# Optimization experiments

Hardware: AMD Instinct MI355X
Metric: run time of the kernel (lower is better)

## Reference

```python
import jax, jax.numpy as jnp
import numpy as np

VW, VD, VH = 96, 96, 96  # voxel_width, voxel_depth, voxel_height


def _grid_points():
    # voxel centers mapped to [-1, 1]: (2*i + 1 - N) / N
    xp = (2.0 * jnp.arange(VW) + 1.0 - VW) / VW
    yp = (2.0 * jnp.arange(VD) + 1.0 - VD) / VD
    zp = (2.0 * jnp.arange(VH) + 1.0 - VH) / VH
    X, Y, Z = jnp.meshgrid(xp, yp, zp, indexing='ij')
    return jnp.stack([X.ravel(), Y.ravel(), Z.ravel()], axis=-1)  # (V, 3)


def setup_inputs() -> dict:
    key = jax.random.key(0)
    k1, k2 = jax.random.split(key)
    B, NV, NF = 8, 2048, 512
    vertices = jax.random.uniform(k1, (B, NV, 3), dtype=jnp.float32, minval=-1.0, maxval=1.0)
    facets = jax.random.randint(k2, (B, NF, 4), 0, NV, dtype=jnp.int64)
    return {"vertices": vertices, "facets": facets}


def reference(vertices, facets):
    # vertices: (B, NV, 3) float32; facets: (B, NF, 4) int indices into vertices
    B = vertices.shape[0]
    NF = facets.shape[1]
    # vertices_to_facets: per-batch gather -> (B, NF, 4, 3)
    fverts = jax.vmap(lambda v, f: v[f])(vertices, facets)
    P = _grid_points()                      # (V, 3) voxel centers
    V = P.shape[0]

    def step(idx_map, xs):
        fi, verts = xs                      # verts: (B, 4, 3)
        v3 = verts[:, 3]                    # (B, 3)
        # T[:, j] = verts[j] - verts[3]  (columns are tetra edges)
        T = jnp.swapaxes(verts[:, :3] - v3[:, None, :], 1, 2)  # (B, 3, 3)
        a, b, c = T[:, 0, 0], T[:, 0, 1], T[:, 0, 2]
        d, e, f = T[:, 1, 0], T[:, 1, 1], T[:, 1, 2]
        g, h, i = T[:, 2, 0], T[:, 2, 1], T[:, 2, 2]
        # adjugate of T (matches t_inv_* in the original)
        adj = jnp.stack([
            jnp.stack([e * i - f * h, c * h - b * i, b * f - c * e], axis=-1),
            jnp.stack([f * g - d * i, a * i - c * g, c * d - a * f], axis=-1),
            jnp.stack([d * h - e * g, b * g - a * h, a * e - b * d], axis=-1),
        ], axis=1)                          # (B, 3, 3)
        det = a * (e * i - f * h) - b * (d * i - f * g) + c * (d * h - e * g)  # (B,)
        dvec = P[None, :, :] - v3[:, None, :]                  # (B, V, 3)
        lam = jnp.einsum('brc,bvc->bvr', adj, dvec) / det[:, None, None]  # (B, V, 3)
        lam4 = 1.0 - lam.sum(axis=-1, keepdims=True)
        lams = jnp.concatenate([lam, lam4], axis=-1)           # (B, V, 4)
        # original skips when any lambda < 0 or > 1 (strict) -> inside is inclusive
        inside = jnp.all((lams >= 0.0) & (lams <= 1.0), axis=-1)  # (B, V)
        idx_map = jnp.where((idx_map < 0) & inside, fi, idx_map)
        return idx_map, None

    idx0 = jnp.full((B, V), -1, dtype=jnp.int32)
    xs = (jnp.arange(NF, dtype=jnp.int32), jnp.swapaxes(fverts, 0, 1))
    idx_map, _ = jax.lax.scan(step, idx0, xs)
    alpha = (idx_map >= 0).astype(jnp.float32).reshape(B, VW, VD, VH)
    return alpha
```

## Files before the change

kernel.cpp:

```cpp
#include <hip/hip_runtime.h>

#pragma clang fp contract(off)

#define VWD 96
#define NVERT 2048
#define NFAC 512
#define NBATCH 8
#define NSLAB 3456
#define RECF 16
#define CULC 22

#define CUL(c, b, f) cul[(size_t)(c) * (NBATCH * NFAC) + (size_t)(b) * NFAC + (f)]

__global__ __launch_bounds__(512) void precompute_kernel(
    const float* __restrict__ vertices,
    const int*   __restrict__ facets,
    float*       __restrict__ cul,
    float*       __restrict__ body)
{
    __shared__ unsigned skey[NFAC];
    const int b = blockIdx.x;
    const int j = threadIdx.x;
    const float* vb = vertices + (size_t)b * NVERT * 3;

    int4 fi = ((const int4*)facets)[b * NFAC + j];
    float x0 = vb[3*fi.x+0], y0 = vb[3*fi.x+1], z0 = vb[3*fi.x+2];
    float x1 = vb[3*fi.y+0], y1 = vb[3*fi.y+1], z1 = vb[3*fi.y+2];
    float x2 = vb[3*fi.z+0], y2 = vb[3*fi.z+1], z2 = vb[3*fi.z+2];
    float x3 = vb[3*fi.w+0], y3 = vb[3*fi.w+1], z3 = vb[3*fi.w+2];
    float a  = x0-x3, bb = x1-x3, c  = x2-x3;
    float d  = y0-y3, e  = y1-y3, f  = y2-y3;
    float g  = z0-z3, h  = z1-z3, ii = z2-z3;
    float A00 = e*ii - f*h,  A01 = c*h  - bb*ii, A02 = bb*f - c*e;
    float A10 = f*g  - d*ii, A11 = a*ii - c*g,   A12 = c*d  - a*f;
    float A20 = d*h  - e*g,  A21 = bb*g - a*h,   A22 = a*e  - bb*d;
    float det = a*(e*ii - f*h) - bb*(d*ii - f*g) + c*(d*h - e*g);
    if (det < 0.0f) {
        det = -det;
        A00 = -A00; A01 = -A01; A02 = -A02;
        A10 = -A10; A11 = -A11; A12 = -A12;
        A20 = -A20; A21 = -A21; A22 = -A22;
    }
    unsigned myk = ~__float_as_uint(det);
    skey[j] = myk;
    __syncthreads();

    int rank = 0;
    const uint4* sk4 = (const uint4*)skey;
    for (int k0 = 0; k0 < NFAC; k0 += 4) {
        uint4 kk = sk4[k0 >> 2];
        rank += (kk.x < myk) + ((kk.x == myk) & (k0 + 0 < j));
        rank += (kk.y < myk) + ((kk.y == myk) & (k0 + 1 < j));
        rank += (kk.z < myk) + ((kk.z == myk) & (k0 + 2 < j));
        rank += (kk.w < myk) + ((kk.w == myk) & (k0 + 3 < j));
    }

    CUL(0, b, rank) = fminf(fminf(x0,x1),fminf(x2,x3)) - 1e-4f;
    CUL(1, b, rank) = fminf(fminf(y0,y1),fminf(y2,y3)) - 1e-4f;
    CUL(2, b, rank) = fminf(fminf(z0,z1),fminf(z2,z3)) - 1e-4f;
    CUL(3, b, rank) = fmaxf(fmaxf(x0,x1),fmaxf(x2,x3)) + 1e-4f;
    CUL(4, b, rank) = fmaxf(fmaxf(y0,y1),fmaxf(y2,y3)) + 1e-4f;
    CUL(5, b, rank) = fmaxf(fmaxf(z0,z1),fmaxf(z2,z3)) + 1e-4f;

    const float HX = 7.0f/96.0f, HZ = 3.0f/96.0f;
    auto plane = [&](float pax, float pay, float paz,
                     float pbx, float pby, float pbz,
                     float pcx, float pcy, float pcz,
                     float pox, float poy, float poz, int base) {
        float e1x = pbx-pax, e1y = pby-pay, e1z = pbz-paz;
        float e2x = pcx-pax, e2y = pcy-pay, e2z = pcz-paz;
        float nx = e1y*e2z - e1z*e2y;
        float ny = e1z*e2x - e1x*e2z;
        float nz = e1x*e2y - e1y*e2x;
        float sdot = nx*(pox-pax) + ny*(poy-pay) + nz*(poz-paz);
        if (sdot > 0.0f) { nx=-nx; ny=-ny; nz=-nz; sdot=-sdot; }
        float dpl = nx*pax + ny*pay + nz*paz;
        float n1s = fabsf(nx)+fabsf(ny)+fabsf(nz);
        float M = 1e-4f*(-sdot) + 1e-4f*n1s + 1e-4f;
        float rhs = dpl + M + (fabsf(nx)*HX + fabsf(ny)*HX + fabsf(nz)*HZ);
        CUL(base+0, b, rank) = nx;
        CUL(base+1, b, rank) = ny;
        CUL(base+2, b, rank) = nz;
        CUL(base+3, b, rank) = rhs;
    };
    plane(x1,y1,z1, x2,y2,z2, x3,y3,z3, x0,y0,z0, 6);
    plane(x0,y0,z0, x2,y2,z2, x3,y3,z3, x1,y1,z1, 10);
    plane(x0,y0,z0, x1,y1,z1, x3,y3,z3, x2,y2,z2, 14);
    plane(x0,y0,z0, x1,y1,z1, x2,y2,z2, x3,y3,z3, 18);

    float* bo = body + ((size_t)b * NFAC + rank) * RECF;
    bo[0]  = det; bo[1]  = x3;  bo[2]  = y3;  bo[3]  = z3;
    bo[4]  = A00; bo[5]  = A01; bo[6]  = A02;
    bo[7]  = A10; bo[8]  = A11; bo[9]  = A12;
    bo[10] = A20; bo[11] = A21; bo[12] = A22;
    bo[13] = det * (1.0f - 1e-5f) - 1e-25f;
    bo[14] = det * (1.0f + 1e-5f) + 1e-25f;
    bo[15] = 0.0f;
}

__global__ __launch_bounds__(512) void mask_kernel(
    const float* __restrict__ cul,
    unsigned long long* __restrict__ masks)
{
    const int col = blockIdx.x;
    const int b   = blockIdx.y;
    const int f   = threadIdx.x;
    const int w   = threadIdx.x >> 6;
    float bminx=CUL(0,b,f), bminy=CUL(1,b,f), bminz=CUL(2,b,f);
    float bmaxx=CUL(3,b,f), bmaxy=CUL(4,b,f), bmaxz=CUL(5,b,f);
    float n0x=CUL(6,b,f),  n0y=CUL(7,b,f),  n0z=CUL(8,b,f),  r0=CUL(9,b,f);
    float n1x=CUL(10,b,f), n1y=CUL(11,b,f), n1z=CUL(12,b,f), r1=CUL(13,b,f);
    float n2x=CUL(14,b,f), n2y=CUL(15,b,f), n2z=CUL(16,b,f), r2=CUL(17,b,f);
    float n3x=CUL(18,b,f), n3y=CUL(19,b,f), n3z=CUL(20,b,f), r3=CUL(21,b,f);

    const int sx = col / 12, sy = col % 12;
    const float cx = (float)(16*sx + 8 - VWD) / 96.0f;
    const float cy = (float)(16*sy + 8 - VWD) / 96.0f;
    const float colminx = (float)(16*sx + 1  - VWD) / 96.0f;
    const float colmaxx = (float)(16*sx + 15 - VWD) / 96.0f;
    const float colminy = (float)(16*sy + 1  - VWD) / 96.0f;
    const float colmaxy = (float)(16*sy + 15 - VWD) / 96.0f;
    const bool ovxy = (bminx <= colmaxx) & (bmaxx >= colminx) &
                      (bminy <= colmaxy) & (bmaxy >= colminy);

    const float cz0   = (float)(4 - VWD) / 96.0f;
    const float stepc = 8.0f / 96.0f;
    float d0 = n0x*cx + n0y*cy + n0z*cz0 - r0;  float s0 = n0z*stepc;
    float d1 = n1x*cx + n1y*cy + n1z*cz0 - r1;  float s1 = n1z*stepc;
    float d2 = n2x*cx + n2y*cy + n2z*cz0 - r2;  float s2 = n2z*stepc;
    float d3 = n3x*cx + n3y*cy + n3z*cz0 - r3;  float s3 = n3z*stepc;
    float zlo = (float)(1 - VWD) / 96.0f;
    float zhi = (float)(7 - VWD) / 96.0f;

    unsigned long long* mp = masks + ((size_t)b * NSLAB + (size_t)col * 24) * 8 + w;
#pragma unroll 4
    for (int sz = 0; sz < 24; ++sz) {
        bool ov = ovxy & (bminz <= zhi) & (bmaxz >= zlo) &
                  (d0 <= 0.0f) & (d1 <= 0.0f) & (d2 <= 0.0f) & (d3 <= 0.0f);
        unsigned long long bal = __ballot((int)ov);
        if ((threadIdx.x & 63) == 0) mp[(size_t)sz * 8] = bal;
        d0 += s0; d1 += s1; d2 += s2; d3 += s3;
        zlo += stepc; zhi += stepc;
    }
}

__global__ __launch_bounds__(256) void voxelize_kernel(
    const float*              __restrict__ body,
    const unsigned long long* __restrict__ masks,
    float*                    __restrict__ out)
{
    const int b    = blockIdx.y;
    const int wave = threadIdx.x >> 6;
    const int lane = threadIdx.x & 63;
    const int slab = blockIdx.x * 4 + wave;
    const int sz = slab % 24;
    const int sy = (slab / 24) % 12;
    const int sx = slab / 288;
    const int ix  = sx*8 + (lane >> 3);
    const int iy  = sy*8 + (lane & 7);
    const int iz0 = sz*4;

    const float px  = (float)(2*ix + 1 - VWD) / 96.0f;
    const float py  = (float)(2*iy + 1 - VWD) / 96.0f;
    const float pz0 = (float)(2*(iz0+0) + 1 - VWD) / 96.0f;
    const float pz1 = (float)(2*(iz0+1) + 1 - VWD) / 96.0f;
    const float pz2 = (float)(2*(iz0+2) + 1 - VWD) / 96.0f;
    const float pz3 = (float)(2*(iz0+3) + 1 - VWD) / 96.0f;

    const unsigned long long* mp = masks + ((size_t)b * NSLAB + slab) * 8;
    const float* bb = body + (size_t)b * NFAC * RECF;

    unsigned fnd = 0u;
    for (int w = 0; w < 8; ++w) {
        unsigned long long m = mp[w];
        while (m) {
            int bit = __builtin_ctzll(m);
            m &= m - 1;
            int f = __builtin_amdgcn_readfirstlane(w * 64 + bit);
            const float* bo = bb + f * RECF;
            float det = bo[0], v3x = bo[1], v3y = bo[2], v3z = bo[3];
            float A00 = bo[4],  A01 = bo[5],  A02 = bo[6];
            float A10 = bo[7],  A11 = bo[8],  A12 = bo[9];
            float A20 = bo[10], A21 = bo[11], A22 = bo[12];
            float dhi = bo[13], mhi = bo[14];
            float dx = px - v3x, dy = py - v3y;
            float p0 = A00*dx + A01*dy;
            float p1 = A10*dx + A11*dy;
            float p2 = A20*dx + A21*dy;
            float dzk0 = pz0 - v3z, dzk1 = pz1 - v3z;
            float dzk2 = pz2 - v3z, dzk3 = pz3 - v3z;
#pragma unroll
            for (int k = 0; k < 4; ++k) {
                float dzk = (k == 0) ? dzk0 : (k == 1) ? dzk1
                          : (k == 2) ? dzk2 : dzk3;
                float n0 = p0 + A02*dzk;
                float n1 = p1 + A12*dzk;
                float n2 = p2 + A22*dzk;
                float sm = (n0 + n1) + n2;
                float mn = fminf(fminf(n0, n1), n2);
                bool ge0 = (mn >= 0.0f);
                bool def = ge0 & (sm <= dhi);
                bool may = ge0 & (sm <= mhi);
                bool needex = may & !def & !((fnd >> k) & 1u);
                if (__any(needex)) {
                    float l0 = n0 / det;
                    float l1 = n1 / det;
                    float l2 = n2 / det;
                    float l3 = 1.0f - ((l0 + l1) + l2);
                    bool inside = (l0 >= 0.0f) & (l0 <= 1.0f) &
                                  (l1 >= 0.0f) & (l1 <= 1.0f) &
                                  (l2 >= 0.0f) & (l2 <= 1.0f) &
                                  (l3 >= 0.0f) & (l3 <= 1.0f);
                    if (needex & inside) fnd |= (1u << k);
                }
                if (def) fnd |= (1u << k);
            }
            if (__all(fnd == 15u)) goto done;
        }
    }
done:
    float4 v;
    v.x = (fnd & 1u) ? 1.0f : 0.0f;
    v.y = (fnd & 2u) ? 1.0f : 0.0f;
    v.z = (fnd & 4u) ? 1.0f : 0.0f;
    v.w = (fnd & 8u) ? 1.0f : 0.0f;
    *(float4*)&out[(size_t)b*(VWD*VWD*VWD) + (size_t)ix*(VWD*VWD) + iy*VWD + iz0] = v;
}

extern "C" void kernel_launch(void* const* d_in, const int* in_sizes, int n_in,
                              void* d_out, int out_size, void* d_ws, size_t ws_size,
                              hipStream_t stream) {
    const float* vertices = (const float*)d_in[0];
    const int*   facets   = (const int*)d_in[1];
    float*       out      = (float*)d_out;

    float* cul  = (float*)d_ws;
    float* body = (float*)((char*)d_ws + (size_t)CULC * NBATCH * NFAC * 4);
    unsigned long long* msk =
        (unsigned long long*)((char*)d_ws +
                              (size_t)(CULC + RECF) * NBATCH * NFAC * 4);

    precompute_kernel<<<NBATCH, 512, 0, stream>>>(vertices, facets, cul, body);
    mask_kernel<<<dim3(144, NBATCH), 512, 0, stream>>>(cul, msk);
    dim3 grid(NSLAB / 4, NBATCH);
    voxelize_kernel<<<grid, 256, 0, stream>>>(body, msk, out);
}
```

Before: 145.8 us.

## Use persistent voxelize blocks with atomic work-stealing over slab chunks

Replaces the static one-wave-per-slab grid with a fixed grid of 2048 blocks whose waves fetch groups of four slabs from a global atomic counter, reset by the precompute kernel. The goal is to even out load across compute units, since slabs differ widely in how many candidate facets they test. The cost is one atomic per four slabs, extra workspace for the counter, and a dependence on the counter being reset before each launch.

```diff
diff --git a/kernel.cpp b/kernel.cpp
--- a/kernel.cpp
+++ b/kernel.cpp
@@ -7,6 +7,8 @@
 #define NFAC 512
 #define NBATCH 8
 #define NSLAB 3456
+#define NWORK (NSLAB * NBATCH)
+#define GRAIN 4
 #define RECF 16
 #define CULC 22
 
@@ -16,11 +18,13 @@
     const float* __restrict__ vertices,
     const int*   __restrict__ facets,
     float*       __restrict__ cul,
-    float*       __restrict__ body)
+    float*       __restrict__ body,
+    unsigned*    __restrict__ counter)
 {
     __shared__ unsigned skey[NFAC];
     const int b = blockIdx.x;
     const int j = threadIdx.x;
+    if (b == 0 && j == 0) *counter = 0u;
     const float* vb = vertices + (size_t)b * NVERT * 3;
 
     int4 fi = ((const int4*)facets)[b * NFAC + j];
@@ -147,84 +151,98 @@
 __global__ __launch_bounds__(256) void voxelize_kernel(
     const float*              __restrict__ body,
     const unsigned long long* __restrict__ masks,
-    float*                    __restrict__ out)
+    float*                    __restrict__ out,
+    unsigned*                 __restrict__ counter)
 {
-    const int b    = blockIdx.y;
-    const int wave = threadIdx.x >> 6;
     const int lane = threadIdx.x & 63;
-    const int slab = blockIdx.x * 4 + wave;
-    const int sz = slab % 24;
-    const int sy = (slab / 24) % 12;
-    const int sx = slab / 288;
-    const int ix  = sx*8 + (lane >> 3);
-    const int iy  = sy*8 + (lane & 7);
-    const int iz0 = sz*4;
-
-    const float px  = (float)(2*ix + 1 - VWD) / 96.0f;
-    const float py  = (float)(2*iy + 1 - VWD) / 96.0f;
-    const float pz0 = (float)(2*(iz0+0) + 1 - VWD) / 96.0f;
-    const float pz1 = (float)(2*(iz0+1) + 1 - VWD) / 96.0f;
-    const float pz2 = (float)(2*(iz0+2) + 1 - VWD) / 96.0f;
-    const float pz3 = (float)(2*(iz0+3) + 1 - VWD) / 96.0f;
-
-    const unsigned long long* mp = masks + ((size_t)b * NSLAB + slab) * 8;
-    const float* bb = body + (size_t)b * NFAC * RECF;
-
-    unsigned fnd = 0u;
-    for (int w = 0; w < 8; ++w) {
-        unsigned long long m = mp[w];
-        while (m) {
-            int bit = __builtin_ctzll(m);
-            m &= m - 1;
-            int f = __builtin_amdgcn_readfirstlane(w * 64 + bit);
-            const float* bo = bb + f * RECF;
-            float det = bo[0], v3x = bo[1], v3y = bo[2], v3z = bo[3];
-            float A00 = bo[4],  A01 = bo[5],  A02 = bo[6];
-            float A10 = bo[7],  A11 = bo[8],  A12 = bo[9];
-            float A20 = bo[10], A21 = bo[11], A22 = bo[12];
-            float dhi = bo[13], mhi = bo[14];
-            float dx = px - v3x, dy = py - v3y;
-            float p0 = A00*dx + A01*dy;
-            float p1 = A10*dx + A11*dy;
-            float p2 = A20*dx + A21*dy;
-            float dzk0 = pz0 - v3z, dzk1 = pz1 - v3z;
-            float dzk2 = pz2 - v3z, dzk3 = pz3 - v3z;
+
+    for (;;) {
+        unsigned g;
+        if (lane == 0) g = atomicAdd(counter, 1u);
+        g = (unsigned)__builtin_amdgcn_readfirstlane((int)g);
+        if (g >= NWORK / GRAIN) return;
+
+        for (int t = 0; t < GRAIN; ++t) {
+            const unsigned id = g * GRAIN + t;
+            const int b    = id / NSLAB;
+            const int slab = id % NSLAB;
+            const int sz = slab % 24;
+            const int sy = (slab / 24) % 12;
+            const int sx = slab / 288;
+            const int ix  = sx*8 + (lane >> 3);
+            const int iy  = sy*8 + (lane & 7);
+            const int iz0 = sz*4;
+
+            const float px  = (float)(2*ix + 1 - VWD) / 96.0f;
+            const float py  = (float)(2*iy + 1 - VWD) / 96.0f;
+            const float pz0 = (float)(2*(iz0+0) + 1 - VWD) / 96.0f;
+            const float pz1 = (float)(2*(iz0+1) + 1 - VWD) / 96.0f;
+            const float pz2 = (float)(2*(iz0+2) + 1 - VWD) / 96.0f;
+            const float pz3 = (float)(2*(iz0+3) + 1 - VWD) / 96.0f;
+
+            const unsigned long long* mp = masks + ((size_t)b * NSLAB + slab) * 8;
+            const float* bb = body + (size_t)b * NFAC * RECF;
+
+            unsigned fnd = 0u;
+            for (int w = 0; w < 8; ++w) {
+                unsigned long long m = mp[w];
+                while (m) {
+                    int bit = __builtin_ctzll(m);
+                    m &= m - 1;
+                    int f = __builtin_amdgcn_readfirstlane(w * 64 + bit);
+                    const float* bo = bb + f * RECF;
+                    float det = bo[0], v3x = bo[1], v3y = bo[2], v3z = bo[3];
+                    float A00 = bo[4],  A01 = bo[5],  A02 = bo[6];
+                    float A10 = bo[7],  A11 = bo[8],  A12 = bo[9];
+                    float A20 = bo[10], A21 = bo[11], A22 = bo[12];
+                    float dhi = bo[13], mhi = bo[14];
+                    float dx = px - v3x, dy = py - v3y;
+                    float p0 = A00*dx + A01*dy;
+                    float p1 = A10*dx + A11*dy;
+                    float p2 = A20*dx + A21*dy;
+                    float dzk0 = pz0 - v3z, dzk1 = pz1 - v3z;
+                    float dzk2 = pz2 - v3z, dzk3 = pz3 - v3z;
 #pragma unroll
-            for (int k = 0; k < 4; ++k) {
-                float dzk = (k == 0) ? dzk0 : (k == 1) ? dzk1
-                          : (k == 2) ? dzk2 : dzk3;
-                float n0 = p0 + A02*dzk;
-                float n1 = p1 + A12*dzk;
-                float n2 = p2 + A22*dzk;
-                float sm = (n0 + n1) + n2;
-                float mn = fminf(fminf(n0, n1), n2);
-                bool ge0 = (mn >= 0.0f);
-                bool def = ge0 & (sm <= dhi);
-                bool may = ge0 & (sm <= mhi);
-                bool needex = may & !def & !((fnd >> k) & 1u);
-                if (__any(needex)) {
-                    float l0 = n0 / det;
-                    float l1 = n1 / det;
-                    float l2 = n2 / det;
-                    float l3 = 1.0f - ((l0 + l1) + l2);
-                    bool inside = (l0 >= 0.0f) & (l0 <= 1.0f) &
-                                  (l1 >= 0.0f) & (l1 <= 1.0f) &
-                                  (l2 >= 0.0f) & (l2 <= 1.0f) &
-                                  (l3 >= 0.0f) & (l3 <= 1.0f);
-                    if (needex & inside) fnd |= (1u << k);
+                    for (int k = 0; k < 4; ++k) {
+                        float dzk = (k == 0) ? dzk0 : (k == 1) ? dzk1
+                                  : (k == 2) ? dzk2 : dzk3;
+                        float n0 = p0 + A02*dzk;
+                        float n1 = p1 + A12*dzk;
+                        float n2 = p2 + A22*dzk;
+                        float sm = (n0 + n1) + n2;
+                        float mn = fminf(fminf(n0, n1), n2);
+                        bool ge0 = (mn >= 0.0f);
+                        bool def = ge0 & (sm <= dhi);
+                        bool may = ge0 & (sm <= mhi);
+                        bool needex = may & !def & !((fnd >> k) & 1u);
+                        if (__any(needex)) {
+                            float l0 = n0 / det;
+                            float l1 = n1 / det;
+                            float l2 = n2 / det;
+                            float l3 = 1.0f - ((l0 + l1) + l2);
+                            bool inside = (l0 >= 0.0f) & (l0 <= 1.0f) &
+                                          (l1 >= 0.0f) & (l1 <= 1.0f) &
+                                          (l2 >= 0.0f) & (l2 <= 1.0f) &
+                                          (l3 >= 0.0f) & (l3 <= 1.0f);
+                            if (needex & inside) fnd |= (1u << k);
+                        }
+                        if (def) fnd |= (1u << k);
+                    }
+                    if (__all(fnd == 15u)) goto slab_done;
                 }
-                if (def) fnd |= (1u << k);
             }
-            if (__all(fnd == 15u)) goto done;
+slab_done:
+            {
+                float4 v;
+                v.x = (fnd & 1u) ? 1.0f : 0.0f;
+                v.y = (fnd & 2u) ? 1.0f : 0.0f;
+                v.z = (fnd & 4u) ? 1.0f : 0.0f;
+                v.w = (fnd & 8u) ? 1.0f : 0.0f;
+                *(float4*)&out[(size_t)b*(VWD*VWD*VWD)
+                               + (size_t)ix*(VWD*VWD) + iy*VWD + iz0] = v;
+            }
         }
     }
-done:
-    float4 v;
-    v.x = (fnd & 1u) ? 1.0f : 0.0f;
-    v.y = (fnd & 2u) ? 1.0f : 0.0f;
-    v.z = (fnd & 4u) ? 1.0f : 0.0f;
-    v.w = (fnd & 8u) ? 1.0f : 0.0f;
-    *(float4*)&out[(size_t)b*(VWD*VWD*VWD) + (size_t)ix*(VWD*VWD) + iy*VWD + iz0] = v;
 }
 
 extern "C" void kernel_launch(void* const* d_in, const int* in_sizes, int n_in,
@@ -236,12 +254,12 @@
 
     float* cul  = (float*)d_ws;
     float* body = (float*)((char*)d_ws + (size_t)CULC * NBATCH * NFAC * 4);
-    unsigned long long* msk =
-        (unsigned long long*)((char*)d_ws +
-                              (size_t)(CULC + RECF) * NBATCH * NFAC * 4);
-
-    precompute_kernel<<<NBATCH, 512, 0, stream>>>(vertices, facets, cul, body);
+    char*  after_body = (char*)d_ws + (size_t)(CULC + RECF) * NBATCH * NFAC * 4;
+    unsigned long long* msk = (unsigned long long*)after_body;
+    unsigned* counter =
+        (unsigned*)(after_body + (size_t)NBATCH * NSLAB * 8 * sizeof(unsigned long long));
+
+    precompute_kernel<<<NBATCH, 512, 0, stream>>>(vertices, facets, cul, body, counter);
     mask_kernel<<<dim3(144, NBATCH), 512, 0, stream>>>(cul, msk);
-    dim3 grid(NSLAB / 4, NBATCH);
-    voxelize_kernel<<<grid, 256, 0, stream>>>(body, msk, out);
-}
+    voxelize_kernel<<<2048, 256, 0, stream>>>(body, msk, out, counter);
+}
```

Result: slower. 287.2 us (+97.0%).
